# Kernel tuning notes

Measured on AMD Instinct MI355X. Metric: run time of the kernel, lower is better.

## Reference

```python
import jax, jax.numpy as jnp
import numpy as np

V_NT, V_RULE, E, H = 200, 500, 1024, 1024  # H == E so cat([nt_emb, prod_emb]) == E + H
B, T, L_NL, L_ENV = 32, 128, 512, 512


def setup_inputs() -> dict:
    key = jax.random.key(0)
    ks = jax.random.split(key, 20)
    s = 0.02
    return {
        'init_prod': jax.random.randint(ks[0], (B,), 0, V_RULE),
        'nt_ids': jax.random.randint(ks[1], (T, B), 0, V_NT),
        'h0': jax.random.normal(ks[2], (B, H), jnp.float32),
        'c0': jax.random.normal(ks[3], (B, H), jnp.float32),
        'nl_encoding': jax.random.normal(ks[4], (B, L_NL, H), jnp.float32),
        'env_encoding': jax.random.normal(ks[5], (B, L_ENV, H), jnp.float32),
        'nt_emb': jax.random.normal(ks[6], (V_NT, E), jnp.float32) * s,
        'rule_emb': jax.random.normal(ks[7], (V_RULE, E), jnp.float32) * s,
        'W_ih': jax.random.normal(ks[8], (4 * H, E + H), jnp.float32) * s,
        'W_hh': jax.random.normal(ks[9], (4 * H, H), jnp.float32) * s,
        'b_ih': jnp.zeros((4 * H,), jnp.float32),
        'b_hh': jnp.zeros((4 * H,), jnp.float32),
        'Wz': jax.random.normal(ks[10], (H, 2 * H), jnp.float32) * s,
        'bz': jnp.zeros((H,), jnp.float32),
        'We': jax.random.normal(ks[11], (H, 2 * H), jnp.float32) * s,
        'be': jnp.zeros((H,), jnp.float32),
        'Wc': jax.random.normal(ks[12], (H, 3 * H), jnp.float32) * s,
        'bc': jnp.zeros((H,), jnp.float32),
    }


def _attention(query, context, W, b):
    # query: (B, H), context: (B, L, H)
    scores = jnp.einsum('bh,blh->bl', query, context)          # bmm(output, context^T)
    attn = jax.nn.softmax(scores, axis=-1)                     # softmax over input_len
    mix = jnp.einsum('bl,blh->bh', attn, context)              # bmm(attn, context)
    out = jnp.tanh(jnp.concatenate([mix, query], axis=-1) @ W.T + b)
    return out, attn


def reference(init_prod, nt_ids, h0, c0, nl_encoding, env_encoding,
              nt_emb, rule_emb, W_ih, W_hh, b_ih, b_hh,
              Wz, bz, We, be, Wc, bc):
    last_prod = rule_emb[init_prod]  # (B, E); never updated in the source loop

    def step(carry, nt_t):
        h, c = carry
        x = jnp.concatenate([nt_emb[nt_t], last_prod], axis=-1)  # (B, E+H)
        gates = x @ W_ih.T + b_ih + h @ W_hh.T + b_hh             # (B, 4H)
        i, f, g, o = jnp.split(gates, 4, axis=-1)                 # torch gate order i,f,g,o
        i = jax.nn.sigmoid(i); f = jax.nn.sigmoid(f)
        g = jnp.tanh(g); o = jax.nn.sigmoid(o)
        c_new = f * c + i * g
        h_new = o * jnp.tanh(c_new)
        st = h_new                                                # (B, H)
        zt, _ = _attention(st, nl_encoding, Wz, bz)               # nl cross-attention
        et, _ = _attention(zt, env_encoding, We, be)              # env cross-attention
        ct = jnp.tanh(jnp.concatenate([st, zt, et], axis=-1) @ Wc.T + bc)
        return (h_new, c_new), ct

    _, cts = jax.lax.scan(step, (h0, c0), nt_ids)  # cts: (T, B, H)
    return cts
```

## Files before the change

kernel.cpp:

```cpp
#include <hip/hip_runtime.h>
#include <hip/hip_bf16.h>

typedef _Float16 f16;
typedef __attribute__((ext_vector_type(8))) _Float16 f16x8;
typedef __attribute__((ext_vector_type(4))) float f32x4;

#define TT 128
#define LSTM_BLOCKS 128

__device__ __forceinline__ float sigmoidf_(float x) { return 1.0f / (1.0f + __expf(-x)); }

__global__ __launch_bounds__(256) void k_f2h(const float* __restrict__ in,
                                             f16* __restrict__ out, long n4) {
  long i = (long)blockIdx.x * 256 + threadIdx.x;
  if (i >= n4) return;
  float4 v = ((const float4*)in)[i];
  out[i*4+0] = (f16)v.x; out[i*4+1] = (f16)v.y;
  out[i*4+2] = (f16)v.z; out[i*4+3] = (f16)v.w;
}

__global__ __launch_bounds__(256) void k_gather_prod(const float* __restrict__ rule_emb,
                                                     const int* __restrict__ init_prod,
                                                     f16* __restrict__ out) {
  int i = blockIdx.x * 256 + threadIdx.x;
  int b = i >> 10, k = i & 1023;
  out[i] = (f16)rule_emb[(long)init_prod[b] * 1024 + k];
}

__global__ __launch_bounds__(256) void k_h0(const float* __restrict__ h0,
                                            f16* __restrict__ st) {
  int i = blockIdx.x * 256 + threadIdx.x;
  int b = i >> 10, k = i & 1023;
  st[(long)b * 129 * 1024 + k] = (f16)h0[i];
}

__global__ __launch_bounds__(256) void k_zero(int* p, int n) {
  for (int i = threadIdx.x; i < n; i += 256) p[i] = 0;
}

__global__ __launch_bounds__(256) void k_transpose(const float* __restrict__ in,
                                                   f16* __restrict__ outT,
                                                   f16* __restrict__ outN) {
  __shared__ float tile[32][33];
  const int b  = blockIdx.z;
  const int l0 = blockIdx.x * 32, h0 = blockIdx.y * 32;
  in   += (long)b * 512 * 1024;
  outT += (long)b * 1024 * 512;
  outN += (long)b * 512 * 1024;
  const int c = threadIdx.x & 31, r = threadIdx.x >> 5;
#pragma unroll
  for (int p = 0; p < 4; ++p) {
    float v = in[(long)(l0 + r + p*8) * 1024 + h0 + c];
    tile[r + p*8][c] = v;
    outN[(long)(l0 + r + p*8) * 1024 + h0 + c] = (f16)v;
  }
  __syncthreads();
#pragma unroll
  for (int p = 0; p < 4; ++p)
    outT[(long)(h0 + r + p*8) * 512 + l0 + c] = (f16)tile[c][r + p*8];
}

__global__ __launch_bounds__(256) void k_gemm(
    const f16* __restrict__ A, long lda, long sA,
    const f16* __restrict__ B, long ldb, long sB,
    float* __restrict__ outF, long ldF, long sF, long sSl,
    f16* __restrict__ outH, long ldH, long sH,
    f16* __restrict__ outH2, long ldH2, long sH2,
    f16* __restrict__ out2, long ld2, long s2,
    const float* __restrict__ bias1, const float* __restrict__ bias2,
    int M, int N, int K, int act, int bmod, int zdiv, int ilv)
{
  __shared__ __align__(16) f16 As[128][40];
  __shared__ __align__(16) f16 Bs[128][40];
  const int tid = threadIdx.x;
  const int w = tid >> 6, lane = tid & 63;
  const int wm = (w & 1) * 64, wn = (w >> 1) * 64;
  const int lr = lane >> 4, lc = lane & 15;
  const long m0 = (long)blockIdx.x * 128;
  const long n0 = (long)blockIdx.y * 128;
  int z = blockIdx.z, batch = z, slice = 0, Ks = K;
  if (zdiv > 1) { batch = z / zdiv; slice = z - batch * zdiv; Ks = K / zdiv; }
  const long kbeg = (long)slice * Ks;
  A += (long)batch * sA;
  B += (long)batch * sB;

  const int rr = tid >> 2, sg = (tid & 3) * 8;
  const int nIt = Ks / 32;

  uint4 pa[2], pb[2];
  {
    long k = kbeg;
    long kb = bmod ? (k & (bmod - 1)) : k;
#pragma unroll
    for (int p = 0; p < 2; ++p) {
      int row = p * 64 + rr;
      uint4 va = {0,0,0,0}, vb = {0,0,0,0};
      if (m0 + row < M) va = *(const uint4*)(A + (m0 + row) * lda + k + sg);
      if (n0 + row < N) vb = *(const uint4*)(B + (n0 + row) * ldb + kb + sg);
      pa[p] = va; pb[p] = vb;
    }
  }

  f32x4 acc[4][4];
#pragma unroll
  for (int i = 0; i < 4; ++i)
#pragma unroll
    for (int j = 0; j < 4; ++j) { f32x4 zz = {0.f,0.f,0.f,0.f}; acc[i][j] = zz; }

  for (int it = 0; it < nIt; ++it) {
#pragma unroll
    for (int p = 0; p < 2; ++p) {
      *(uint4*)&As[p * 64 + rr][sg] = pa[p];
      *(uint4*)&Bs[p * 64 + rr][sg] = pb[p];
    }
    __syncthreads();
    if (it + 1 < nIt) {
      long k = kbeg + (long)(it + 1) * 32;
      long kb = bmod ? (k & (bmod - 1)) : k;
#pragma unroll
      for (int p = 0; p < 2; ++p) {
        int row = p * 64 + rr;
        uint4 va = {0,0,0,0}, vb = {0,0,0,0};
        if (m0 + row < M) va = *(const uint4*)(A + (m0 + row) * lda + k + sg);
        if (n0 + row < N) vb = *(const uint4*)(B + (n0 + row) * ldb + kb + sg);
        pa[p] = va; pb[p] = vb;
      }
    }
    f16x8 af[4], bf[4];
#pragma unroll
    for (int i = 0; i < 4; ++i) af[i] = *(const f16x8*)&As[wm + i*16 + lc][lr * 8];
#pragma unroll
    for (int j = 0; j < 4; ++j) bf[j] = *(const f16x8*)&Bs[wn + j*16 + lc][lr * 8];
#pragma unroll
    for (int i = 0; i < 4; ++i)
#pragma unroll
      for (int j = 0; j < 4; ++j)
        acc[i][j] = __builtin_amdgcn_mfma_f32_16x16x32_f16(af[i], bf[j], acc[i][j], 0, 0, 0);
    __syncthreads();
  }

  if (outF)  outF  += (long)batch * sF + (long)slice * sSl;
  if (outH)  outH  += (long)batch * sH;
  if (outH2) outH2 += (long)batch * sH2;
  if (out2)  out2  += (long)batch * s2;
#pragma unroll
  for (int i = 0; i < 4; ++i)
#pragma unroll
    for (int j = 0; j < 4; ++j)
#pragma unroll
      for (int r = 0; r < 4; ++r) {
        long row = m0 + wm + i * 16 + lr * 4 + r;
        long col = n0 + wn + j * 16 + lc;
        if (row < M && col < N) {
          float v = acc[i][j][r];
          if (bias1) v += bias1[col];
          if (bias2) v += bias2[col];
          if (act)   v = tanhf(v);
          if (outF) {
            long fc = ilv ? ((col & 1023) * 4 + (col >> 10)) : col;
            outF[row * ldF + fc] = v;
          }
          if (outH)  outH[row * ldH + col] = (f16)v;
          if (outH2) outH2[row * ldH2 + col] = (f16)v;
          if (out2) {
            f16 hi = (f16)v;
            out2[row * ld2 + col]        = hi;
            out2[row * ld2 + 1024 + col] = (f16)(v - (float)hi);
          }
        }
      }
}

__global__ __launch_bounds__(256) void k_lstm_all(
    const f16* __restrict__ Whh,
    const float* __restrict__ nt_table,
    const float* __restrict__ prod_gates,
    const int* __restrict__ nt_ids,
    const float* __restrict__ c0,
    f16* __restrict__ st,
    f16* __restrict__ q2,
    f16* __restrict__ X,
    f16* __restrict__ Y1,
    int* __restrict__ flags)
{
  __shared__ __align__(16) f16 whh_s[32][1032];
  __shared__ float partial[4][32][34];
  const int tid = threadIdx.x;
  const int w = tid >> 6, lane = tid & 63;
  const int lr = lane >> 4, lc = lane & 15;
  const int j0 = blockIdx.x * 8;

  for (int i = tid; i < 32 * 128; i += 256) {
    int r = i >> 7, c8 = i & 127;
    int g = r >> 3, jj = r & 7;
    *(uint4*)&whh_s[r][c8 * 8] =
        *(const uint4*)(Whh + ((long)g * 1024 + j0 + jj) * 1024 + c8 * 8);
  }
  const int b_own = tid >> 3, jj_own = tid & 7;
  const int j_own = j0 + jj_own;
  float c_reg = c0[(long)b_own * 1024 + j_own];
  float4 pg4 = *(const float4*)(prod_gates + (long)b_own * 4096 + j_own * 4);
  int nid0 = nt_ids[b_own];
  float4 nt4 = *(const float4*)(nt_table + (long)nid0 * 4096 + j_own * 4);

  const f16* pa0 = st + (long)lc * (129 * 1024) + w * 256 + lr * 8;
  const f16* pa1 = pa0 + 16L * 129 * 1024;

  __syncthreads();

  for (int t = 0; t < TT; ++t) {
    f16x8 a0[8], a1[8];
#pragma unroll
    for (int kt = 0; kt < 8; ++kt) {
      a0[kt] = *(const f16x8*)(pa0 + (long)t * 1024 + kt * 32);
      a1[kt] = *(const f16x8*)(pa1 + (long)t * 1024 + kt * 32);
    }
    float4 nt4n = nt4;
    if (t + 1 < TT) {
      int nidn = nt_ids[(t + 1) * 32 + b_own];
      nt4n = *(const float4*)(nt_table + (long)nidn * 4096 + j_own * 4);
    }

    f32x4 acc[2][2];
#pragma unroll
    for (int i = 0; i < 2; ++i)
#pragma unroll
      for (int j = 0; j < 2; ++j) { f32x4 zz = {0.f,0.f,0.f,0.f}; acc[i][j] = zz; }
#pragma unroll
    for (int kt = 0; kt < 8; ++kt) {
      int k = w * 256 + kt * 32 + lr * 8;
      f16x8 b0 = *(const f16x8*)&whh_s[lc][k];
      f16x8 b1 = *(const f16x8*)&whh_s[16 + lc][k];
      acc[0][0] = __builtin_amdgcn_mfma_f32_16x16x32_f16(a0[kt], b0, acc[0][0], 0, 0, 0);
      acc[0][1] = __builtin_amdgcn_mfma_f32_16x16x32_f16(a0[kt], b1, acc[0][1], 0, 0, 0);
      acc[1][0] = __builtin_amdgcn_mfma_f32_16x16x32_f16(a1[kt], b0, acc[1][0], 0, 0, 0);
      acc[1][1] = __builtin_amdgcn_mfma_f32_16x16x32_f16(a1[kt], b1, acc[1][1], 0, 0, 0);
    }
#pragma unroll
    for (int mi = 0; mi < 2; ++mi)
#pragma unroll
      for (int ni = 0; ni < 2; ++ni)
#pragma unroll
        for (int r = 0; r < 4; ++r)
          partial[w][ni * 16 + lc][mi * 16 + lr * 4 + r] = acc[mi][ni][r];
    __syncthreads();

    float g4[4];
#pragma unroll
    for (int g = 0; g < 4; ++g) {
      int rrow = g * 8 + jj_own;
      g4[g] = partial[0][rrow][b_own] + partial[1][rrow][b_own] +
              partial[2][rrow][b_own] + partial[3][rrow][b_own];
    }
    float ii = sigmoidf_(g4[0] + nt4.x + pg4.x);
    float ff = sigmoidf_(g4[1] + nt4.y + pg4.y);
    float gg = tanhf(g4[2] + nt4.z + pg4.z);
    float oo = sigmoidf_(g4[3] + nt4.w + pg4.w);
    c_reg = ff * c_reg + ii * gg;
    float hn = oo * tanhf(c_reg);
    f16 hi = (f16)hn;

    if (t + 1 < TT) {
      union { f16 h; unsigned short u; } cv; cv.h = hi;
      unsigned v32 = cv.u;
      const f16* pst = st + ((long)b_own * 129 + t + 1) * 1024 + j_own;
      asm volatile("global_store_short %0, %1, off sc0 sc1\n\t"
                   "s_waitcnt vmcnt(0)" :: "v"(pst), "v"(v32) : "memory");
      __syncthreads();
      if (tid == 0)
        __hip_atomic_store(&flags[blockIdx.x * 32], t + 1,
                           __ATOMIC_RELAXED, __HIP_MEMORY_SCOPE_AGENT);
    }

    long row = (long)b_own * 128 + t;
    q2[row * 2048 + j_own]        = hi;
    q2[row * 2048 + 1024 + j_own] = (f16)(hn - (float)hi);
    X[row * 3072 + j_own]         = hi;
    Y1[row * 2048 + 1024 + j_own] = hi;

    if (t + 1 < TT) {
      if (tid < 64) {
        int* f0p = &flags[(2 * tid) * 32];
        int* f1p = &flags[(2 * tid + 1) * 32];
        int done = 0;
        while (true) {
          if (!done) {
            int a = __hip_atomic_load(f0p, __ATOMIC_RELAXED, __HIP_MEMORY_SCOPE_AGENT);
            int b = __hip_atomic_load(f1p, __ATOMIC_RELAXED, __HIP_MEMORY_SCOPE_AGENT);
            done = (a > t) & (b > t);
          }
          if (__all(done)) break;
          __builtin_amdgcn_s_sleep(2);
        }
      }
      __syncthreads();
      asm volatile("" ::: "memory");
    }
    nt4 = nt4n;
  }
}

__global__ __launch_bounds__(256) void k_softmax4(const float* __restrict__ p,
                                                  long pstride,
                                                  f16* __restrict__ out) {
  long row = blockIdx.x;
  const float* p0 = p + row * 512;
  out += row * 512;
  const int tid = threadIdx.x, w = tid >> 6, lane = tid & 63;
  float vx = 0.f, vy = 0.f;
#pragma unroll
  for (int s = 0; s < 4; ++s) {
    float2 a = ((const float2*)(p0 + s * pstride))[tid];
    vx += a.x; vy += a.y;
  }
  float m = fmaxf(vx, vy);
#pragma unroll
  for (int off = 32; off; off >>= 1) m = fmaxf(m, __shfl_xor(m, off));
  __shared__ float red[8];
  if (lane == 0) red[w] = m;
  __syncthreads();
  m = fmaxf(fmaxf(red[0], red[1]), fmaxf(red[2], red[3]));
  float e0 = __expf(vx - m), e1 = __expf(vy - m);
  float s2 = e0 + e1;
#pragma unroll
  for (int off = 32; off; off >>= 1) s2 += __shfl_xor(s2, off);
  if (lane == 0) red[4 + w] = s2;
  __syncthreads();
  s2 = red[4] + red[5] + red[6] + red[7];
  float inv = 1.0f / s2;
  out[tid * 2]     = (f16)(e0 * inv);
  out[tid * 2 + 1] = (f16)(e1 * inv);
}

extern "C" void kernel_launch(void* const* d_in, const int* in_sizes, int n_in,
                              void* d_out, int out_size, void* d_ws, size_t ws_size,
                              hipStream_t stream)
{
  const int*   init_prod = (const int*)d_in[0];
  const int*   nt_ids    = (const int*)d_in[1];
  const float* h0   = (const float*)d_in[2];
  const float* c0   = (const float*)d_in[3];
  const float* nl   = (const float*)d_in[4];
  const float* env  = (const float*)d_in[5];
  const float* nt_emb   = (const float*)d_in[6];
  const float* rule_emb = (const float*)d_in[7];
  const float* W_ih = (const float*)d_in[8];
  const float* W_hh = (const float*)d_in[9];
  const float* b_ih = (const float*)d_in[10];
  const float* b_hh = (const float*)d_in[11];
  const float* Wz   = (const float*)d_in[12];
  const float* bz   = (const float*)d_in[13];
  const float* We   = (const float*)d_in[14];
  const float* be   = (const float*)d_in[15];
  const float* Wc   = (const float*)d_in[16];
  const float* bc   = (const float*)d_in[17];
  float* out = (float*)d_out;
  (void)in_sizes; (void)n_in; (void)out_size; (void)ws_size;

  size_t off = 0;
  auto carve = [&](size_t bytes) {
    char* p = (char*)d_ws + off;
    off += (bytes + 255) & ~(size_t)255;
    return (void*)p;
  };
  f16*   Whh_h   = (f16*)carve(4096L * 1024 * 2);
  f16*   Wz_h    = (f16*)carve(1024L * 2048 * 2);
  f16*   We_h    = (f16*)carve(1024L * 2048 * 2);
  f16*   Wc_h    = (f16*)carve(1024L * 3072 * 2);
  f16*   nte_h   = (f16*)carve(200L * 1024 * 2);
  f16*   prod_h  = (f16*)carve(32L * 1024 * 2);
  float* nt_table   = (float*)carve(200L * 4096 * 4);
  float* prod_gates = (float*)carve(32L * 4096 * 4);
  f16*   st_hi   = (f16*)carve(32L * 129 * 1024 * 2);
  f16*   q2      = (f16*)carve(4096L * 2048 * 2);
  f16*   X       = (f16*)carve(4096L * 3072 * 2);
  f16*   Y1      = (f16*)carve(4096L * 2048 * 2);
  f16*   Y2      = (f16*)carve(4096L * 2048 * 2);
  f16*   ctx_h   = (f16*)carve(32L * 512 * 1024 * 2);
  f16*   ctxT    = (f16*)carve(32L * 1024 * 512 * 2);
  float* scoresP = (float*)carve(4L * 32 * 128 * 512 * 4);
  f16*   attn    = (f16*)carve(4096L * 512 * 2);
  int*   bar     = (int*)carve(16384);
  f16*   Wih_h   = (f16*)X;

  auto f2h = [&](const float* src, f16* dst, long n) {
    long n4 = n / 4;
    k_f2h<<<dim3((unsigned)((n4 + 255) / 256)), dim3(256), 0, stream>>>(src, dst, n4);
  };
  f2h(W_ih, Wih_h, 4096L * 2048);
  f2h(W_hh, Whh_h, 4096L * 1024);
  f2h(Wz,   Wz_h,  1024L * 2048);
  f2h(We,   We_h,  1024L * 2048);
  f2h(Wc,   Wc_h,  1024L * 3072);
  f2h(nt_emb, nte_h, 200L * 1024);
  k_gather_prod<<<dim3(128), dim3(256), 0, stream>>>(rule_emb, init_prod, prod_h);
  k_h0<<<dim3(128), dim3(256), 0, stream>>>(h0, st_hi);
  k_zero<<<dim3(1), dim3(256), 0, stream>>>(bar, 4096);

  auto gemm = [&](const f16* A, long lda, long sA,
                  const f16* B, long ldb, long sB,
                  float* oF, long ldF, long sF, long sSl,
                  f16* oH, long ldH, long sH,
                  f16* oH2, long ldH2, long sH2,
                  f16* o2, long ld2, long s2,
                  const float* b1, const float* b2,
                  int M, int N, int K, int act, int bmod, int zdiv, int ilv,
                  int batch) {
    dim3 grid((unsigned)((M + 127) / 128), (unsigned)((N + 127) / 128),
              (unsigned)(batch * zdiv));
    k_gemm<<<grid, dim3(256), 0, stream>>>(A, lda, sA, B, ldb, sB,
                                           oF, ldF, sF, sSl, oH, ldH, sH,
                                           oH2, ldH2, sH2, o2, ld2, s2,
                                           b1, b2, M, N, K, act, bmod, zdiv, ilv);
  };
  const long SPL = 32L * 128 * 512;

  gemm(nte_h, 1024, 0, Wih_h, 2048, 0, nt_table, 4096, 0, 0,
       nullptr,0,0, nullptr,0,0, nullptr,0,0, nullptr, nullptr,
       200, 4096, 1024, 0, 0, 1, 1, 1);
  gemm(prod_h, 1024, 0, Wih_h + 1024, 2048, 0, prod_gates, 4096, 0, 0,
       nullptr,0,0, nullptr,0,0, nullptr,0,0, b_ih, b_hh,
       32, 4096, 1024, 0, 0, 1, 1, 1);

  k_lstm_all<<<dim3(LSTM_BLOCKS), dim3(256), 0, stream>>>(
      Whh_h, nt_table, prod_gates, nt_ids, c0, st_hi, q2, X, Y1, bar);

  k_transpose<<<dim3(16, 32, 32), dim3(256), 0, stream>>>(nl, ctxT, ctx_h);
  gemm(q2, 2048, 128L * 2048, ctx_h, 1024, 512L * 1024,
       scoresP, 512, 128L * 512, SPL, nullptr,0,0, nullptr,0,0, nullptr,0,0,
       nullptr, nullptr, 128, 512, 2048, 0, 1024, 4, 0, 32);
  k_softmax4<<<dim3(4096), dim3(256), 0, stream>>>(scoresP, SPL, attn);
  gemm(attn, 512, 128L * 512, ctxT, 512, 1024L * 512,
       nullptr,0,0,0, Y1, 2048, 128L * 2048, nullptr,0,0, nullptr,0,0,
       nullptr, nullptr, 128, 1024, 512, 0, 0, 1, 0, 32);
  gemm(Y1, 2048, 0, Wz_h, 2048, 0,
       nullptr,0,0,0, X + 1024, 3072, 0, Y2 + 1024, 2048, 0, q2, 2048, 0,
       bz, nullptr, 4096, 1024, 2048, 1, 0, 1, 0, 1);

  k_transpose<<<dim3(16, 32, 32), dim3(256), 0, stream>>>(env, ctxT, ctx_h);
  gemm(q2, 2048, 128L * 2048, ctx_h, 1024, 512L * 1024,
       scoresP, 512, 128L * 512, SPL, nullptr,0,0, nullptr,0,0, nullptr,0,0,
       nullptr, nullptr, 128, 512, 2048, 0, 1024, 4, 0, 32);
  k_softmax4<<<dim3(4096), dim3(256), 0, stream>>>(scoresP, SPL, attn);
  gemm(attn, 512, 128L * 512, ctxT, 512, 1024L * 512,
       nullptr,0,0,0, Y2, 2048, 128L * 2048, nullptr,0,0, nullptr,0,0,
       nullptr, nullptr, 128, 1024, 512, 0, 0, 1, 0, 32);
  gemm(Y2, 2048, 0, We_h, 2048, 0,
       nullptr,0,0,0, X + 2048, 3072, 0, nullptr,0,0, nullptr,0,0,
       be, nullptr, 4096, 1024, 2048, 1, 0, 1, 0, 1);

  gemm(X, 3072, 128L * 3072, Wc_h, 3072, 0,
       out, 32L * 1024, 1024, 0, nullptr,0,0, nullptr,0,0, nullptr,0,0,
       bc, nullptr, 128, 1024, 3072, 1, 0, 1, 0, 32);
}
```

Baseline: 1.249 ms.

## Replace flag-based grid barrier in LSTM with poisoned-data polling

Removes the per-step flag store and the cross-block flag spin barrier from the persistent LSTM kernel. The hidden-state buffer is instead pre-filled with 0xFFFF (a NaN f16 pattern), and each wave polls its own A-operand loads until no poisoned halfwords remain, so readiness is detected directly from the data. This cuts a store-wait, a block barrier and a flag round-trip from each timestep. In exchange it adds a poison-fill kernel over the state buffer, relies on the computed f16 hidden value never being the 0xFFFF NaN pattern, and depends on the ordering of individual 2-byte stores.

```diff
diff --git a/kernel.cpp b/kernel.cpp
--- a/kernel.cpp
+++ b/kernel.cpp
@@ -4,6 +4,7 @@
 typedef _Float16 f16;
 typedef __attribute__((ext_vector_type(8))) _Float16 f16x8;
 typedef __attribute__((ext_vector_type(4))) float f32x4;
+typedef __attribute__((ext_vector_type(4))) unsigned int u32x4;
 
 #define TT 128
 #define LSTM_BLOCKS 128
@@ -27,15 +28,16 @@
   out[i] = (f16)rule_emb[(long)init_prod[b] * 1024 + k];
 }
 
+__global__ __launch_bounds__(256) void k_poison(unsigned int* __restrict__ p, long n) {
+  long i = (long)blockIdx.x * 256 + threadIdx.x;
+  if (i < n) p[i] = 0xFFFFFFFFu;
+}
+
 __global__ __launch_bounds__(256) void k_h0(const float* __restrict__ h0,
                                             f16* __restrict__ st) {
   int i = blockIdx.x * 256 + threadIdx.x;
   int b = i >> 10, k = i & 1023;
   st[(long)b * 129 * 1024 + k] = (f16)h0[i];
-}
-
-__global__ __launch_bounds__(256) void k_zero(int* p, int n) {
-  for (int i = threadIdx.x; i < n; i += 256) p[i] = 0;
 }
 
 __global__ __launch_bounds__(256) void k_transpose(const float* __restrict__ in,
@@ -180,8 +182,7 @@
     f16* __restrict__ st,
     f16* __restrict__ q2,
     f16* __restrict__ X,
-    f16* __restrict__ Y1,
-    int* __restrict__ flags)
+    f16* __restrict__ Y1)
 {
   __shared__ __align__(16) f16 whh_s[32][1032];
   __shared__ float partial[4][32][34];
@@ -208,13 +209,54 @@
 
   __syncthreads();
 
+#define PKMAX(acc_, v_) asm("v_pk_max_u16 %0, %0, %1" : "+v"(acc_) : "v"(v_))
+
   for (int t = 0; t < TT; ++t) {
-    f16x8 a0[8], a1[8];
-#pragma unroll
-    for (int kt = 0; kt < 8; ++kt) {
-      a0[kt] = *(const f16x8*)(pa0 + (long)t * 1024 + kt * 32);
-      a1[kt] = *(const f16x8*)(pa1 + (long)t * 1024 + kt * 32);
-    }
+    u32x4 A0[8], A1[8];
+    const f16* p0 = pa0 + (long)t * 1024;
+    const f16* p1 = pa1 + (long)t * 1024;
+    int done = 0;
+    while (true) {
+      if (!done) {
+        asm volatile(
+          "global_load_dwordx4 %0, %16, off sc0 sc1\n\t"
+          "global_load_dwordx4 %1, %16, off offset:64 sc0 sc1\n\t"
+          "global_load_dwordx4 %2, %16, off offset:128 sc0 sc1\n\t"
+          "global_load_dwordx4 %3, %16, off offset:192 sc0 sc1\n\t"
+          "global_load_dwordx4 %4, %16, off offset:256 sc0 sc1\n\t"
+          "global_load_dwordx4 %5, %16, off offset:320 sc0 sc1\n\t"
+          "global_load_dwordx4 %6, %16, off offset:384 sc0 sc1\n\t"
+          "global_load_dwordx4 %7, %16, off offset:448 sc0 sc1\n\t"
+          "global_load_dwordx4 %8, %17, off sc0 sc1\n\t"
+          "global_load_dwordx4 %9, %17, off offset:64 sc0 sc1\n\t"
+          "global_load_dwordx4 %10, %17, off offset:128 sc0 sc1\n\t"
+          "global_load_dwordx4 %11, %17, off offset:192 sc0 sc1\n\t"
+          "global_load_dwordx4 %12, %17, off offset:256 sc0 sc1\n\t"
+          "global_load_dwordx4 %13, %17, off offset:320 sc0 sc1\n\t"
+          "global_load_dwordx4 %14, %17, off offset:384 sc0 sc1\n\t"
+          "global_load_dwordx4 %15, %17, off offset:448 sc0 sc1\n\t"
+          "s_waitcnt vmcnt(0)"
+          : "=&v"(A0[0]), "=&v"(A0[1]), "=&v"(A0[2]), "=&v"(A0[3]),
+            "=&v"(A0[4]), "=&v"(A0[5]), "=&v"(A0[6]), "=&v"(A0[7]),
+            "=&v"(A1[0]), "=&v"(A1[1]), "=&v"(A1[2]), "=&v"(A1[3]),
+            "=&v"(A1[4]), "=&v"(A1[5]), "=&v"(A1[6]), "=&v"(A1[7])
+          : "v"(p0), "v"(p1)
+          : "memory");
+        unsigned mA = 0, mB = 0, mC = 0, mD = 0;
+#pragma unroll
+        for (int kt = 0; kt < 8; ++kt) {
+          PKMAX(mA, A0[kt].x); PKMAX(mB, A0[kt].y);
+          PKMAX(mC, A0[kt].z); PKMAX(mD, A0[kt].w);
+          PKMAX(mA, A1[kt].x); PKMAX(mB, A1[kt].y);
+          PKMAX(mC, A1[kt].z); PKMAX(mD, A1[kt].w);
+        }
+        PKMAX(mA, mB); PKMAX(mC, mD); PKMAX(mA, mC);
+        done = !(((mA & 0xFFFFu) == 0xFFFFu) || ((mA >> 16) == 0xFFFFu));
+      }
+      if (__all(done)) break;
+      __builtin_amdgcn_s_sleep(2);
+    }
+
     float4 nt4n = nt4;
     if (t + 1 < TT) {
       int nidn = nt_ids[(t + 1) * 32 + b_own];
@@ -228,13 +270,15 @@
       for (int j = 0; j < 2; ++j) { f32x4 zz = {0.f,0.f,0.f,0.f}; acc[i][j] = zz; }
 #pragma unroll
     for (int kt = 0; kt < 8; ++kt) {
+      f16x8 a0v = __builtin_bit_cast(f16x8, A0[kt]);
+      f16x8 a1v = __builtin_bit_cast(f16x8, A1[kt]);
       int k = w * 256 + kt * 32 + lr * 8;
       f16x8 b0 = *(const f16x8*)&whh_s[lc][k];
       f16x8 b1 = *(const f16x8*)&whh_s[16 + lc][k];
-      acc[0][0] = __builtin_amdgcn_mfma_f32_16x16x32_f16(a0[kt], b0, acc[0][0], 0, 0, 0);
-      acc[0][1] = __builtin_amdgcn_mfma_f32_16x16x32_f16(a0[kt], b1, acc[0][1], 0, 0, 0);
-      acc[1][0] = __builtin_amdgcn_mfma_f32_16x16x32_f16(a1[kt], b0, acc[1][0], 0, 0, 0);
-      acc[1][1] = __builtin_amdgcn_mfma_f32_16x16x32_f16(a1[kt], b1, acc[1][1], 0, 0, 0);
+      acc[0][0] = __builtin_amdgcn_mfma_f32_16x16x32_f16(a0v, b0, acc[0][0], 0, 0, 0);
+      acc[0][1] = __builtin_amdgcn_mfma_f32_16x16x32_f16(a0v, b1, acc[0][1], 0, 0, 0);
+      acc[1][0] = __builtin_amdgcn_mfma_f32_16x16x32_f16(a1v, b0, acc[1][0], 0, 0, 0);
+      acc[1][1] = __builtin_amdgcn_mfma_f32_16x16x32_f16(a1v, b1, acc[1][1], 0, 0, 0);
     }
 #pragma unroll
     for (int mi = 0; mi < 2; ++mi)
@@ -252,6 +296,8 @@
       g4[g] = partial[0][rrow][b_own] + partial[1][rrow][b_own] +
               partial[2][rrow][b_own] + partial[3][rrow][b_own];
     }
+    __syncthreads();
+
     float ii = sigmoidf_(g4[0] + nt4.x + pg4.x);
     float ff = sigmoidf_(g4[1] + nt4.y + pg4.y);
     float gg = tanhf(g4[2] + nt4.z + pg4.z);
@@ -264,12 +310,8 @@
       union { f16 h; unsigned short u; } cv; cv.h = hi;
       unsigned v32 = cv.u;
       const f16* pst = st + ((long)b_own * 129 + t + 1) * 1024 + j_own;
-      asm volatile("global_store_short %0, %1, off sc0 sc1\n\t"
-                   "s_waitcnt vmcnt(0)" :: "v"(pst), "v"(v32) : "memory");
-      __syncthreads();
-      if (tid == 0)
-        __hip_atomic_store(&flags[blockIdx.x * 32], t + 1,
-                           __ATOMIC_RELAXED, __HIP_MEMORY_SCOPE_AGENT);
+      asm volatile("global_store_short %0, %1, off sc0 sc1"
+                   :: "v"(pst), "v"(v32) : "memory");
     }
 
     long row = (long)b_own * 128 + t;
@@ -278,26 +320,9 @@
     X[row * 3072 + j_own]         = hi;
     Y1[row * 2048 + 1024 + j_own] = hi;
 
-    if (t + 1 < TT) {
-      if (tid < 64) {
-        int* f0p = &flags[(2 * tid) * 32];
-        int* f1p = &flags[(2 * tid + 1) * 32];
-        int done = 0;
-        while (true) {
-          if (!done) {
-            int a = __hip_atomic_load(f0p, __ATOMIC_RELAXED, __HIP_MEMORY_SCOPE_AGENT);
-            int b = __hip_atomic_load(f1p, __ATOMIC_RELAXED, __HIP_MEMORY_SCOPE_AGENT);
-            done = (a > t) & (b > t);
-          }
-          if (__all(done)) break;
-          __builtin_amdgcn_s_sleep(2);
-        }
-      }
-      __syncthreads();
-      asm volatile("" ::: "memory");
-    }
     nt4 = nt4n;
   }
+#undef PKMAX
 }
 
 __global__ __launch_bounds__(256) void k_softmax4(const float* __restrict__ p,
@@ -380,7 +405,6 @@
   f16*   ctxT    = (f16*)carve(32L * 1024 * 512 * 2);
   float* scoresP = (float*)carve(4L * 32 * 128 * 512 * 4);
   f16*   attn    = (f16*)carve(4096L * 512 * 2);
-  int*   bar     = (int*)carve(16384);
   f16*   Wih_h   = (f16*)X;
 
   auto f2h = [&](const float* src, f16* dst, long n) {
@@ -394,8 +418,8 @@
   f2h(Wc,   Wc_h,  1024L * 3072);
   f2h(nt_emb, nte_h, 200L * 1024);
   k_gather_prod<<<dim3(128), dim3(256), 0, stream>>>(rule_emb, init_prod, prod_h);
+  k_poison<<<dim3(8256), dim3(256), 0, stream>>>((unsigned int*)st_hi, 32L * 129 * 512);
   k_h0<<<dim3(128), dim3(256), 0, stream>>>(h0, st_hi);
-  k_zero<<<dim3(1), dim3(256), 0, stream>>>(bar, 4096);
 
   auto gemm = [&](const f16* A, long lda, long sA,
                   const f16* B, long ldb, long sB,
@@ -423,7 +447,7 @@
        32, 4096, 1024, 0, 0, 1, 1, 1);
 
   k_lstm_all<<<dim3(LSTM_BLOCKS), dim3(256), 0, stream>>>(
-      Whh_h, nt_table, prod_gates, nt_ids, c0, st_hi, q2, X, Y1, bar);
+      Whh_h, nt_table, prod_gates, nt_ids, c0, st_hi, q2, X, Y1);
 
   k_transpose<<<dim3(16, 32, 32), dim3(256), 0, stream>>>(nl, ctxT, ctx_h);
   gemm(q2, 2048, 128L * 2048, ctx_h, 1024, 512L * 1024,
```

Measured after the change: 1.263 ms. About the same (+1.1%).

## Restructure LSTM recurrence sync with per-wave flags and blocked h-state layout

Applied to the files above, without the earlier changes.

Changes the persistent LSTM kernel's cross-block synchronization. The single block-wide barrier and polling by wave 0 become per-wave flags, and each wave polls only the flags for the k-slice it consumes. The hidden state is stored in a blocked [k/8][batch][8] layout so each step's A operand is fetched with coalesced dwordx4 loads and written as one 16-byte store per 8 columns. W_hh fragments are hoisted into registers once, and the partial-sum LDS buffer is double-buffered so a barrier can be removed. This cuts per-step latency on the sequential critical path, at the cost of more fine-grained memory-ordering reasoning and higher register pressure.

```diff
diff --git a/kernel.cpp b/kernel.cpp
--- a/kernel.cpp
+++ b/kernel.cpp
@@ -4,6 +4,8 @@
 typedef _Float16 f16;
 typedef __attribute__((ext_vector_type(8))) _Float16 f16x8;
 typedef __attribute__((ext_vector_type(4))) float f32x4;
+typedef __attribute__((ext_vector_type(4))) unsigned int u32x4;
+typedef __attribute__((ext_vector_type(2))) int i32x2;
 
 #define TT 128
 #define LSTM_BLOCKS 128
@@ -31,7 +33,7 @@
                                             f16* __restrict__ st) {
   int i = blockIdx.x * 256 + threadIdx.x;
   int b = i >> 10, k = i & 1023;
-  st[(long)b * 129 * 1024 + k] = (f16)h0[i];
+  st[(long)(k >> 3) * 256 + b * 8 + (k & 7)] = (f16)h0[i];
 }
 
 __global__ __launch_bounds__(256) void k_zero(int* p, int n) {
@@ -171,7 +173,7 @@
       }
 }
 
-__global__ __launch_bounds__(256) void k_lstm_all(
+__global__ __launch_bounds__(256, 1) void k_lstm_all(
     const f16* __restrict__ Whh,
     const float* __restrict__ nt_table,
     const float* __restrict__ prod_gates,
@@ -184,11 +186,12 @@
     int* __restrict__ flags)
 {
   __shared__ __align__(16) f16 whh_s[32][1032];
-  __shared__ float partial[4][32][34];
+  __shared__ float partial[2][4][32][34];
   const int tid = threadIdx.x;
   const int w = tid >> 6, lane = tid & 63;
   const int lr = lane >> 4, lc = lane & 15;
-  const int j0 = blockIdx.x * 8;
+  const int bx = blockIdx.x;
+  const int j0 = bx * 8;
 
   for (int i = tid; i < 32 * 128; i += 256) {
     int r = i >> 7, c8 = i & 127;
@@ -202,19 +205,52 @@
   float4 pg4 = *(const float4*)(prod_gates + (long)b_own * 4096 + j_own * 4);
   int nid0 = nt_ids[b_own];
   float4 nt4 = *(const float4*)(nt_table + (long)nid0 * 4096 + j_own * 4);
-
-  const f16* pa0 = st + (long)lc * (129 * 1024) + w * 256 + lr * 8;
-  const f16* pa1 = pa0 + 16L * 129 * 1024;
-
   __syncthreads();
 
+  f16x8 B0[8], B1[8];
+#pragma unroll
+  for (int kt = 0; kt < 8; ++kt) {
+    int k = w * 256 + kt * 32 + lr * 8;
+    B0[kt] = *(const f16x8*)&whh_s[lc][k];
+    B1[kt] = *(const f16x8*)&whh_s[16 + lc][k];
+  }
+
+  const f16* pA = st + (long)(w * 32 + lr) * 256 + lc * 8;
+  const int* fp = flags + w * 128 + lane * 2;
+
   for (int t = 0; t < TT; ++t) {
-    f16x8 a0[8], a1[8];
-#pragma unroll
-    for (int kt = 0; kt < 8; ++kt) {
-      a0[kt] = *(const f16x8*)(pa0 + (long)t * 1024 + kt * 32);
-      a1[kt] = *(const f16x8*)(pa1 + (long)t * 1024 + kt * 32);
-    }
+    if (t > 0) {
+      int done = 0;
+      while (true) {
+        if (!done) {
+          i32x2 ff;
+          asm volatile("global_load_dwordx2 %0, %1, off sc0 sc1\n\t"
+                       "s_waitcnt vmcnt(0)"
+                       : "=&v"(ff) : "v"(fp) : "memory");
+          done = (ff.x >= t) & (ff.y >= t);
+        }
+        if (__all(done)) break;
+        __builtin_amdgcn_s_sleep(1);
+      }
+    }
+
+    u32x4 A0[8], A1[8];
+    {
+      const f16* pt = pA + (long)t * 32768;
+#pragma unroll
+      for (int q = 0; q < 4; ++q) {
+        asm volatile(
+          "global_load_dwordx4 %0, %4, off sc0 sc1\n\t"
+          "global_load_dwordx4 %1, %4, off offset:256 sc0 sc1\n\t"
+          "global_load_dwordx4 %2, %4, off offset:2048 sc0 sc1\n\t"
+          "global_load_dwordx4 %3, %4, off offset:2304 sc0 sc1"
+          : "=&v"(A0[2*q]), "=&v"(A1[2*q]), "=&v"(A0[2*q+1]), "=&v"(A1[2*q+1])
+          : "v"(pt + (long)q * 2048) : "memory");
+      }
+      asm volatile("s_waitcnt vmcnt(0)" ::: "memory");
+      __builtin_amdgcn_sched_barrier(0);
+    }
+
     float4 nt4n = nt4;
     if (t + 1 < TT) {
       int nidn = nt_ids[(t + 1) * 32 + b_own];
@@ -228,29 +264,29 @@
       for (int j = 0; j < 2; ++j) { f32x4 zz = {0.f,0.f,0.f,0.f}; acc[i][j] = zz; }
 #pragma unroll
     for (int kt = 0; kt < 8; ++kt) {
-      int k = w * 256 + kt * 32 + lr * 8;
-      f16x8 b0 = *(const f16x8*)&whh_s[lc][k];
-      f16x8 b1 = *(const f16x8*)&whh_s[16 + lc][k];
-      acc[0][0] = __builtin_amdgcn_mfma_f32_16x16x32_f16(a0[kt], b0, acc[0][0], 0, 0, 0);
-      acc[0][1] = __builtin_amdgcn_mfma_f32_16x16x32_f16(a0[kt], b1, acc[0][1], 0, 0, 0);
-      acc[1][0] = __builtin_amdgcn_mfma_f32_16x16x32_f16(a1[kt], b0, acc[1][0], 0, 0, 0);
-      acc[1][1] = __builtin_amdgcn_mfma_f32_16x16x32_f16(a1[kt], b1, acc[1][1], 0, 0, 0);
-    }
+      f16x8 a0v = __builtin_bit_cast(f16x8, A0[kt]);
+      f16x8 a1v = __builtin_bit_cast(f16x8, A1[kt]);
+      acc[0][0] = __builtin_amdgcn_mfma_f32_16x16x32_f16(a0v, B0[kt], acc[0][0], 0, 0, 0);
+      acc[0][1] = __builtin_amdgcn_mfma_f32_16x16x32_f16(a0v, B1[kt], acc[0][1], 0, 0, 0);
+      acc[1][0] = __builtin_amdgcn_mfma_f32_16x16x32_f16(a1v, B0[kt], acc[1][0], 0, 0, 0);
+      acc[1][1] = __builtin_amdgcn_mfma_f32_16x16x32_f16(a1v, B1[kt], acc[1][1], 0, 0, 0);
+    }
+    float (*pp)[32][34] = partial[t & 1];
 #pragma unroll
     for (int mi = 0; mi < 2; ++mi)
 #pragma unroll
       for (int ni = 0; ni < 2; ++ni)
 #pragma unroll
         for (int r = 0; r < 4; ++r)
-          partial[w][ni * 16 + lc][mi * 16 + lr * 4 + r] = acc[mi][ni][r];
+          pp[w][ni * 16 + lc][mi * 16 + lr * 4 + r] = acc[mi][ni][r];
     __syncthreads();
 
     float g4[4];
 #pragma unroll
     for (int g = 0; g < 4; ++g) {
       int rrow = g * 8 + jj_own;
-      g4[g] = partial[0][rrow][b_own] + partial[1][rrow][b_own] +
-              partial[2][rrow][b_own] + partial[3][rrow][b_own];
+      g4[g] = pp[0][rrow][b_own] + pp[1][rrow][b_own] +
+              pp[2][rrow][b_own] + pp[3][rrow][b_own];
     }
     float ii = sigmoidf_(g4[0] + nt4.x + pg4.x);
     float ff = sigmoidf_(g4[1] + nt4.y + pg4.y);
@@ -262,14 +298,24 @@
 
     if (t + 1 < TT) {
       union { f16 h; unsigned short u; } cv; cv.h = hi;
-      unsigned v32 = cv.u;
-      const f16* pst = st + ((long)b_own * 129 + t + 1) * 1024 + j_own;
-      asm volatile("global_store_short %0, %1, off sc0 sc1\n\t"
-                   "s_waitcnt vmcnt(0)" :: "v"(pst), "v"(v32) : "memory");
-      __syncthreads();
-      if (tid == 0)
-        __hip_atomic_store(&flags[blockIdx.x * 32], t + 1,
-                           __ATOMIC_RELAXED, __HIP_MEMORY_SCOPE_AGENT);
+      unsigned me = cv.u;
+      unsigned d  = me | ((unsigned)__shfl_down((int)me, 1) << 16);
+      unsigned d2 = (unsigned)__shfl_down((int)d, 2);
+      unsigned e0 = (unsigned)__shfl_down((int)d, 4);
+      unsigned e1 = (unsigned)__shfl_down((int)d2, 4);
+      if (jj_own == 0) {
+        u32x4 pay; pay.x = d; pay.y = d2; pay.z = e0; pay.w = e1;
+        f16* pst = st + (long)(t + 1) * 32768 + bx * 256 + b_own * 8;
+        asm volatile("global_store_dwordx4 %0, %1, off sc0 sc1"
+                     :: "v"(pst), "v"(pay) : "memory");
+      }
+      asm volatile("s_waitcnt vmcnt(0)" ::: "memory");
+      if (lane == 0) {
+        int* myf = flags + bx * 4 + w;
+        int fv = t + 1;
+        asm volatile("global_store_dword %0, %1, off sc0 sc1"
+                     :: "v"(myf), "v"(fv) : "memory");
+      }
     }
 
     long row = (long)b_own * 128 + t;
@@ -278,24 +324,6 @@
     X[row * 3072 + j_own]         = hi;
     Y1[row * 2048 + 1024 + j_own] = hi;
 
-    if (t + 1 < TT) {
-      if (tid < 64) {
-        int* f0p = &flags[(2 * tid) * 32];
-        int* f1p = &flags[(2 * tid + 1) * 32];
-        int done = 0;
-        while (true) {
-          if (!done) {
-            int a = __hip_atomic_load(f0p, __ATOMIC_RELAXED, __HIP_MEMORY_SCOPE_AGENT);
-            int b = __hip_atomic_load(f1p, __ATOMIC_RELAXED, __HIP_MEMORY_SCOPE_AGENT);
-            done = (a > t) & (b > t);
-          }
-          if (__all(done)) break;
-          __builtin_amdgcn_s_sleep(2);
-        }
-      }
-      __syncthreads();
-      asm volatile("" ::: "memory");
-    }
     nt4 = nt4n;
   }
 }
@@ -371,7 +399,7 @@
   f16*   prod_h  = (f16*)carve(32L * 1024 * 2);
   float* nt_table   = (float*)carve(200L * 4096 * 4);
   float* prod_gates = (float*)carve(32L * 4096 * 4);
-  f16*   st_hi   = (f16*)carve(32L * 129 * 1024 * 2);
+  f16*   st_hi   = (f16*)carve(129L * 128 * 32 * 8 * 2);
   f16*   q2      = (f16*)carve(4096L * 2048 * 2);
   f16*   X       = (f16*)carve(4096L * 3072 * 2);
   f16*   Y1      = (f16*)carve(4096L * 2048 * 2);
@@ -380,7 +408,7 @@
   f16*   ctxT    = (f16*)carve(32L * 1024 * 512 * 2);
   float* scoresP = (float*)carve(4L * 32 * 128 * 512 * 4);
   f16*   attn    = (f16*)carve(4096L * 512 * 2);
-  int*   bar     = (int*)carve(16384);
+  int*   bar     = (int*)carve(2048);
   f16*   Wih_h   = (f16*)X;
 
   auto f2h = [&](const float* src, f16* dst, long n) {
@@ -395,7 +423,7 @@
   f2h(nt_emb, nte_h, 200L * 1024);
   k_gather_prod<<<dim3(128), dim3(256), 0, stream>>>(rule_emb, init_prod, prod_h);
   k_h0<<<dim3(128), dim3(256), 0, stream>>>(h0, st_hi);
-  k_zero<<<dim3(1), dim3(256), 0, stream>>>(bar, 4096);
+  k_zero<<<dim3(1), dim3(256), 0, stream>>>(bar, 512);
 
   auto gemm = [&](const f16* A, long lda, long sA,
                   const f16* B, long ldb, long sB,
```

Result: faster. 1.147 ms (-8.1%).
